# Performance work log

Measured on AMD Instinct MI355X. Metric: run time of the kernel, lower is better.

The kernel has to match this reference:

```python
import jax, jax.numpy as jnp
import numpy as np

N, D = 320, 256
TEMP = 2.0

# case ids sorted: [-11,-10,-1,0,1,10,11]; value order: [0,1,2,3,11,12,13]
CASE_VALS = jnp.array([-11, -10, -1, 0, 1, 10, 11], dtype=jnp.int32)
TABLE = jnp.array([
    [0, 2, 2, 1, 1, 0, 1],   # case -11
    [0, 2, 2, 2, 2, 2, 2],   # case -10
    [0, 2, 2, 2, 1, 0, 2],   # case -1
    [0, 2, 2, 2, 2, 2, 2],   # case 0
    [0, 2, 2, 2, 1, 2, 2],   # case 1
    [0, 2, 2, 2, 2, 0, 2],   # case 10
    [0, 2, 2, 1, 1, 0, 1],   # case 11
], dtype=jnp.int32)


def setup_inputs() -> dict:
    key = jax.random.key(0)
    k1, k2, k3 = jax.random.split(key, 3)
    features = jax.random.normal(k1, (N, D), dtype=jnp.float32)
    y_times = jax.random.uniform(k2, (N,), dtype=jnp.float32)
    y_events = jax.random.randint(k3, (N,), 0, 2, dtype=jnp.int32)
    return {"features": features, "y_times": y_times, "y_events": y_events}


def _forward(features, y_times, y_events):
    n = features.shape[0]
    # pairwise -L2 similarity / temperature  (safe sqrt: diag is 0)
    diff = features[:, None, :] - features[None, :, :]          # [N,N,D]
    d2 = jnp.sum(diff * diff, axis=-1)                           # [N,N]
    norm = jnp.where(d2 > 0, jnp.sqrt(jnp.where(d2 > 0, d2, 1.0)), 0.0)
    logits = -norm / TEMP
    logits = logits - jax.lax.stop_gradient(jnp.max(logits, axis=1, keepdims=True))
    exp_logits = jnp.exp(logits)

    idx = jnp.arange(n)
    eye = idx[:, None] == idx[None, :]

    def per_anchor(k):
        pld = y_times - y_times[k]                               # [N]
        abs_i = jnp.abs(pld)[:, None]                            # |pld[i]|
        pj = pld[None, :]                                        # pld[j]
        # sequential torch mask assignments collapse to this piecewise map
        td = jnp.where(pj > abs_i, 3,
             jnp.where(-pj > abs_i, 1,
             jnp.where(jnp.abs(pj) > 0, 2, 0))).astype(jnp.int32)
        td = jnp.where(eye, 0, td)                               # fill_diagonal_(0)
        neg = jnp.where(td != 0, y_events[None, :] * 10 + td, 0) # {0,1,2,3,11,12,13}
        sgn = jnp.sign(pld).astype(jnp.int32)
        cid = (y_events + 10 * y_events[k]) * sgn                # per-row case id
        cidx = jnp.searchsorted(CASE_VALS, cid)                  # [N]
        vidx = jnp.where(neg > 3, neg - 7, neg)                  # map vals to 0..6
        mapped = TABLE[cidx[:, None], vidx]                      # numba lookup, fused
        final = (mapped == 1).astype(jnp.float32) + 0.5 * (mapped == 2)
        keep = (idx != k).astype(jnp.float32)                    # delete row/col k
        final = final * keep[:, None] * keep[None, :]
        valid = jnp.sum(final, axis=-1) > 0                      # [N]
        Np = jnp.sum(valid)
        denom = jnp.sum(final * exp_logits, axis=-1)             # masked sum-exp
        logp = logits[:, k] - jnp.log(jnp.where(valid, denom, 1.0))
        loss_k = -jnp.sum(jnp.where(valid, logp, 0.0)) / jnp.maximum(Np, 1)
        return jnp.where(Np > 0, loss_k, 0.0), (Np > 0)

    losses, has_pos = jax.vmap(per_anchor)(idx)
    return jnp.sum(losses) / jnp.sum(has_pos)


def reference(features, y_times, y_events):
    return _forward(features, y_times, y_events)
```

## Files before the change

kernel.cpp:

```cpp
#include <hip/hip_runtime.h>
#include <math.h>

#define NN 320
#define DD 256

__device__ __constant__ unsigned int c_PACK[7] =
    {0x2294u, 0x1554u, 0x1254u, 0x1554u, 0x1654u, 0x1154u, 0x2294u};

__global__ __launch_bounds__(256) void prep_kernel(
    const float* __restrict__ F, const float* __restrict__ yt,
    const int* __restrict__ ye, float4* __restrict__ FT4,
    float4* __restrict__ meta, float* __restrict__ acc) {
    __shared__ float sh[64 * 65];
    __shared__ int rr[3][4][64];
    const int b = blockIdx.x;
    const int tid = threadIdx.x;
    if (b < 20) {
        float (*tile)[65] = (float(*)[65])sh;
        const int I = b % 5;
        const int J = b / 5;
        const int lane = tid & 63;
        const int quad = tid >> 6;
#pragma unroll
        for (int r0 = 0; r0 < 64; r0 += 4) {
            const int r = r0 + quad;
            tile[r][lane] = F[(I * 64 + r) * DD + J * 64 + lane];
        }
        __syncthreads();
#pragma unroll
        for (int q = 0; q < 16; q += 4) {
            const int d4 = q + quad;
            float4 v = make_float4(tile[lane][d4 * 4 + 0], tile[lane][d4 * 4 + 1],
                                   tile[lane][d4 * 4 + 2], tile[lane][d4 * 4 + 3]);
            FT4[(J * 16 + d4) * NN + I * 64 + lane] = v;
        }
    } else if (b < 25) {
        float* s_t = sh;
        for (int l = tid; l < NN; l += 256) s_t[l] = yt[l];
        __syncthreads();
        const int jj = tid & 63;
        const int q  = tid >> 6;
        const int j  = (b - 20) * 64 + jj;
        const float tj = s_t[j];
        int lt = 0, le = 0, pos = 0;
        const int l0 = q * 80;
        for (int l = l0; l < l0 + 80; ++l) {
            const float tl = s_t[l];
            lt  += (tl < tj);
            le  += (tl <= tj);
            pos += (tl < tj) || (tl == tj && l < j);
        }
        rr[0][q][jj] = lt; rr[1][q][jj] = le; rr[2][q][jj] = pos;
        __syncthreads();
        if (q == 0) {
#pragma unroll
            for (int w = 1; w < 4; ++w) {
                lt += rr[0][w][jj]; le += rr[1][w][jj]; pos += rr[2][w][jj];
            }
            meta[j] = make_float4(tj, __int_as_float(lt), __int_as_float(le),
                                  __int_as_float(pos | (ye[j] << 16)));
        }
    } else {
        for (int t = tid; t < 2 * NN + 1; t += 256) acc[t] = 0.f;
    }
}

__global__ __launch_bounds__(NN) void fused_kernel(
    const float* __restrict__ F, const float4* __restrict__ FT4,
    const float4* __restrict__ meta, float* __restrict__ acc,
    float* __restrict__ out) {
    __shared__ __align__(16) float fi[DD];
    __shared__ float S0[NN + 1];
    __shared__ float S1[NN + 1];
    __shared__ float w0[5], w1[5];
    __shared__ float4 smi;
    __shared__ int s_done;

    float* __restrict__ accL = acc;
    float* __restrict__ accN = acc + NN;
    unsigned* ticket = (unsigned*)(acc + 2 * NN);

    const int i = blockIdx.x;
    const int j = threadIdx.x;
    const int wave = j >> 6, lane = j & 63;

    if (j < DD) fi[j] = F[i * DD + j];
    if (j == 0) smi = meta[i];
    const float4 mj = meta[j];
    __syncthreads();

    const float4* __restrict__ fi4 = (const float4*)fi;
    float a0 = 0.f, a1 = 0.f, a2 = 0.f, a3 = 0.f;
#pragma unroll 8
    for (int d4 = 0; d4 < DD / 4; ++d4) {
        const float4 f4 = fi4[d4];
        const float4 g4 = FT4[d4 * NN + j];
        const float u0 = f4.x - g4.x, u1 = f4.y - g4.y;
        const float u2 = f4.z - g4.z, u3 = f4.w - g4.w;
        a0 = fmaf(u0, u0, a0);
        a1 = fmaf(u1, u1, a1);
        a2 = fmaf(u2, u2, a2);
        a3 = fmaf(u3, u3, a3);
    }
    const float d2 = (a0 + a1) + (a2 + a3);
    const float nrm = (d2 > 0.f) ? sqrtf(d2) : 0.f;
    const float lg = -0.5f * nrm;
    const float e = expf(lg);

    const int pej = __float_as_int(mj.w);
    const int pos = pej & 0xFFFF;
    const int evj = pej >> 16;
    S0[pos] = evj ? 0.f : e;
    S1[pos] = evj ? e : 0.f;
    __syncthreads();

    float v0 = S0[j], v1 = S1[j];
#pragma unroll
    for (int off = 1; off < 64; off <<= 1) {
        const float n0 = __shfl_up(v0, off);
        const float n1 = __shfl_up(v1, off);
        if (lane >= off) { v0 += n0; v1 += n1; }
    }
    if (lane == 63) { w0[wave] = v0; w1[wave] = v1; }
    __syncthreads();
    float p0 = 0.f, p1 = 0.f;
#pragma unroll
    for (int w = 0; w < 4; ++w) {
        if (wave > w) { p0 += w0[w]; p1 += w1[w]; }
    }
    v0 += p0; v1 += p1;
    S0[j + 1] = v0; S1[j + 1] = v1;
    if (j == 0) { S0[0] = 0.f; S1[0] = 0.f; }
    __syncthreads();

    const float4 mi = smi;
    const float ti = mi.x;
    const int rlt_i = __float_as_int(mi.y), rle_i = __float_as_int(mi.z);
    const int evi   = __float_as_int(mi.w) >> 16;
    const float ta = mj.x;
    const int rlt_a = __float_as_int(mj.y), rle_a = __float_as_int(mj.z);
    const int eva   = evj;

    const int sgn = (ti > ta) ? 1 : ((ti < ta) ? -1 : 0);
    const unsigned pack = c_PACK[3 + sgn * (evi + 2 * eva)];
    const int rlo = min(rlt_i, rlt_a);
    const int rhi = max(rle_i, rle_a);

    const float q0lo = S0[rlo], q0hi = S0[rhi], q0a = S0[rlt_a], q0b = S0[rle_a], t0 = S0[NN];
    const float q1lo = S1[rlo], q1hi = S1[rhi], q1a = S1[rlt_a], q1b = S1[rle_a], t1 = S1[NN];

    const float LO0 = q0lo, HI0 = t0 - q0hi, MI0 = q0hi - q0lo - (q0b - q0a);
    const float LO1 = q1lo, HI1 = t1 - q1hi, MI1 = q1hi - q1lo - (q1b - q1a);

    const float c1 = (float)((pack >> 2) & 3u),  c2 = (float)((pack >> 4) & 3u);
    const float c3 = (float)((pack >> 6) & 3u),  c4 = (float)((pack >> 8) & 3u);
    const float c5 = (float)((pack >> 10) & 3u), c6 = (float)((pack >> 12) & 3u);

    float dx = c1 * LO0 + c2 * MI0 + c3 * HI0 + c4 * LO1 + c5 * MI1 + c6 * HI1;
    if (ti != ta) dx -= (float)((pack >> (2 * (2 + 3 * evi))) & 3u);

    if (i != j && dx > 0.f) {
        atomicAdd(&accL[j], lg - logf(0.5f * dx));
        atomicAdd(&accN[j], 1.f);
    }

    __threadfence();
    __syncthreads();
    if (j == 0) {
        const unsigned old = atomicAdd(ticket, 1u);
        s_done = (old == NN - 1);
    }
    __syncthreads();
    if (!s_done) return;
    __threadfence();

    const float nj = accN[j];
    float lossj = (nj > 0.f) ? (-accL[j] / nj) : 0.f;
    float hasj  = (nj > 0.f) ? 1.f : 0.f;
#pragma unroll
    for (int off = 32; off > 0; off >>= 1) {
        lossj += __shfl_down(lossj, off);
        hasj  += __shfl_down(hasj, off);
    }
    if (lane == 0) { w0[wave] = lossj; w1[wave] = hasj; }
    __syncthreads();
    if (j == 0) {
        float tl = 0.f, th = 0.f;
#pragma unroll
        for (int w = 0; w < 5; ++w) { tl += w0[w]; th += w1[w]; }
        out[0] = tl / th;
    }
}

extern "C" void kernel_launch(void* const* d_in, const int* in_sizes, int n_in,
                              void* d_out, int out_size, void* d_ws, size_t ws_size,
                              hipStream_t stream) {
    const float* F  = (const float*)d_in[0];
    const float* yt = (const float*)d_in[1];
    const int*   ye = (const int*)d_in[2];
    float* out = (float*)d_out;
    float* ws  = (float*)d_ws;

    float4* meta = (float4*)ws;
    float4* FT4  = (float4*)(ws + 4 * NN);
    float*  acc  = ws + 4 * NN + 4 * (DD / 4) * NN;

    prep_kernel<<<26, 256, 0, stream>>>(F, yt, ye, FT4, meta, acc);
    fused_kernel<<<NN, NN, 0, stream>>>(F, FT4, meta, acc, out);
}
```

Baseline: 93.71 us.

## Process two anchor rows per block to reuse transposed feature loads

```diff
diff --git a/kernel.cpp b/kernel.cpp
--- a/kernel.cpp
+++ b/kernel.cpp
@@ -69,106 +69,149 @@
     const float* __restrict__ F, const float4* __restrict__ FT4,
     const float4* __restrict__ meta, float* __restrict__ acc,
     float* __restrict__ out) {
-    __shared__ __align__(16) float fi[DD];
-    __shared__ float S0[NN + 1];
-    __shared__ float S1[NN + 1];
-    __shared__ float w0[5], w1[5];
-    __shared__ float4 smi;
+    __shared__ __align__(16) float fiA[DD];
+    __shared__ __align__(16) float fiB[DD];
+    __shared__ float S0A[NN + 1];
+    __shared__ float S1A[NN + 1];
+    __shared__ float S0B[NN + 1];
+    __shared__ float S1B[NN + 1];
+    __shared__ float wv[4][5];
+    __shared__ float4 smiA, smiB;
     __shared__ int s_done;
 
     float* __restrict__ accL = acc;
     float* __restrict__ accN = acc + NN;
     unsigned* ticket = (unsigned*)(acc + 2 * NN);
 
-    const int i = blockIdx.x;
+    const int i0 = blockIdx.x * 2;
+    const int i1 = i0 + 1;
     const int j = threadIdx.x;
     const int wave = j >> 6, lane = j & 63;
 
-    if (j < DD) fi[j] = F[i * DD + j];
-    if (j == 0) smi = meta[i];
+    if (j < DD) {
+        fiA[j] = F[i0 * DD + j];
+        fiB[j] = F[i1 * DD + j];
+    }
+    if (j == 0) smiA = meta[i0];
+    if (j == 1) smiB = meta[i1];
     const float4 mj = meta[j];
     __syncthreads();
 
-    const float4* __restrict__ fi4 = (const float4*)fi;
-    float a0 = 0.f, a1 = 0.f, a2 = 0.f, a3 = 0.f;
+    const float4* __restrict__ fA4 = (const float4*)fiA;
+    const float4* __restrict__ fB4 = (const float4*)fiB;
+    float aA0 = 0.f, aA1 = 0.f, aA2 = 0.f, aA3 = 0.f;
+    float aB0 = 0.f, aB1 = 0.f, aB2 = 0.f, aB3 = 0.f;
 #pragma unroll 8
     for (int d4 = 0; d4 < DD / 4; ++d4) {
-        const float4 f4 = fi4[d4];
         const float4 g4 = FT4[d4 * NN + j];
-        const float u0 = f4.x - g4.x, u1 = f4.y - g4.y;
-        const float u2 = f4.z - g4.z, u3 = f4.w - g4.w;
-        a0 = fmaf(u0, u0, a0);
-        a1 = fmaf(u1, u1, a1);
-        a2 = fmaf(u2, u2, a2);
-        a3 = fmaf(u3, u3, a3);
-    }
-    const float d2 = (a0 + a1) + (a2 + a3);
-    const float nrm = (d2 > 0.f) ? sqrtf(d2) : 0.f;
-    const float lg = -0.5f * nrm;
-    const float e = expf(lg);
+        const float4 fA = fA4[d4];
+        const float4 fB = fB4[d4];
+        float u;
+        u = fA.x - g4.x; aA0 = fmaf(u, u, aA0);
+        u = fA.y - g4.y; aA1 = fmaf(u, u, aA1);
+        u = fA.z - g4.z; aA2 = fmaf(u, u, aA2);
+        u = fA.w - g4.w; aA3 = fmaf(u, u, aA3);
+        u = fB.x - g4.x; aB0 = fmaf(u, u, aB0);
+        u = fB.y - g4.y; aB1 = fmaf(u, u, aB1);
+        u = fB.z - g4.z; aB2 = fmaf(u, u, aB2);
+        u = fB.w - g4.w; aB3 = fmaf(u, u, aB3);
+    }
+    const float d2A = (aA0 + aA1) + (aA2 + aA3);
+    const float d2B = (aB0 + aB1) + (aB2 + aB3);
+    const float lgA = -0.5f * ((d2A > 0.f) ? sqrtf(d2A) : 0.f);
+    const float lgB = -0.5f * ((d2B > 0.f) ? sqrtf(d2B) : 0.f);
+    const float eA = expf(lgA);
+    const float eB = expf(lgB);
 
     const int pej = __float_as_int(mj.w);
     const int pos = pej & 0xFFFF;
     const int evj = pej >> 16;
-    S0[pos] = evj ? 0.f : e;
-    S1[pos] = evj ? e : 0.f;
-    __syncthreads();
-
-    float v0 = S0[j], v1 = S1[j];
+    S0A[pos] = evj ? 0.f : eA;
+    S1A[pos] = evj ? eA : 0.f;
+    S0B[pos] = evj ? 0.f : eB;
+    S1B[pos] = evj ? eB : 0.f;
+    __syncthreads();
+
+    float vA0 = S0A[j], vA1 = S1A[j], vB0 = S0B[j], vB1 = S1B[j];
 #pragma unroll
     for (int off = 1; off < 64; off <<= 1) {
-        const float n0 = __shfl_up(v0, off);
-        const float n1 = __shfl_up(v1, off);
-        if (lane >= off) { v0 += n0; v1 += n1; }
-    }
-    if (lane == 63) { w0[wave] = v0; w1[wave] = v1; }
-    __syncthreads();
-    float p0 = 0.f, p1 = 0.f;
+        const float nA0 = __shfl_up(vA0, off);
+        const float nA1 = __shfl_up(vA1, off);
+        const float nB0 = __shfl_up(vB0, off);
+        const float nB1 = __shfl_up(vB1, off);
+        if (lane >= off) { vA0 += nA0; vA1 += nA1; vB0 += nB0; vB1 += nB1; }
+    }
+    if (lane == 63) {
+        wv[0][wave] = vA0; wv[1][wave] = vA1;
+        wv[2][wave] = vB0; wv[3][wave] = vB1;
+    }
+    __syncthreads();
+    float pA0 = 0.f, pA1 = 0.f, pB0 = 0.f, pB1 = 0.f;
 #pragma unroll
     for (int w = 0; w < 4; ++w) {
-        if (wave > w) { p0 += w0[w]; p1 += w1[w]; }
-    }
-    v0 += p0; v1 += p1;
-    S0[j + 1] = v0; S1[j + 1] = v1;
-    if (j == 0) { S0[0] = 0.f; S1[0] = 0.f; }
-    __syncthreads();
-
-    const float4 mi = smi;
-    const float ti = mi.x;
-    const int rlt_i = __float_as_int(mi.y), rle_i = __float_as_int(mi.z);
-    const int evi   = __float_as_int(mi.w) >> 16;
+        if (wave > w) {
+            pA0 += wv[0][w]; pA1 += wv[1][w];
+            pB0 += wv[2][w]; pB1 += wv[3][w];
+        }
+    }
+    vA0 += pA0; vA1 += pA1; vB0 += pB0; vB1 += pB1;
+    S0A[j + 1] = vA0; S1A[j + 1] = vA1;
+    S0B[j + 1] = vB0; S1B[j + 1] = vB1;
+    if (j == 0) { S0A[0] = 0.f; S1A[0] = 0.f; S0B[0] = 0.f; S1B[0] = 0.f; }
+    __syncthreads();
+
     const float ta = mj.x;
     const int rlt_a = __float_as_int(mj.y), rle_a = __float_as_int(mj.z);
     const int eva   = evj;
 
-    const int sgn = (ti > ta) ? 1 : ((ti < ta) ? -1 : 0);
-    const unsigned pack = c_PACK[3 + sgn * (evi + 2 * eva)];
-    const int rlo = min(rlt_i, rlt_a);
-    const int rhi = max(rle_i, rle_a);
-
-    const float q0lo = S0[rlo], q0hi = S0[rhi], q0a = S0[rlt_a], q0b = S0[rle_a], t0 = S0[NN];
-    const float q1lo = S1[rlo], q1hi = S1[rhi], q1a = S1[rlt_a], q1b = S1[rle_a], t1 = S1[NN];
-
-    const float LO0 = q0lo, HI0 = t0 - q0hi, MI0 = q0hi - q0lo - (q0b - q0a);
-    const float LO1 = q1lo, HI1 = t1 - q1hi, MI1 = q1hi - q1lo - (q1b - q1a);
-
-    const float c1 = (float)((pack >> 2) & 3u),  c2 = (float)((pack >> 4) & 3u);
-    const float c3 = (float)((pack >> 6) & 3u),  c4 = (float)((pack >> 8) & 3u);
-    const float c5 = (float)((pack >> 10) & 3u), c6 = (float)((pack >> 12) & 3u);
-
-    float dx = c1 * LO0 + c2 * MI0 + c3 * HI0 + c4 * LO1 + c5 * MI1 + c6 * HI1;
-    if (ti != ta) dx -= (float)((pack >> (2 * (2 + 3 * evi))) & 3u);
-
-    if (i != j && dx > 0.f) {
-        atomicAdd(&accL[j], lg - logf(0.5f * dx));
-        atomicAdd(&accN[j], 1.f);
+    float lp = 0.f, np = 0.f;
+#pragma unroll
+    for (int r = 0; r < 2; ++r) {
+        const float4 mi = (r == 0) ? smiA : smiB;
+        const float* __restrict__ S0 = (r == 0) ? S0A : S0B;
+        const float* __restrict__ S1 = (r == 0) ? S1A : S1B;
+        const float lg = (r == 0) ? lgA : lgB;
+        const int irow = (r == 0) ? i0 : i1;
+
+        const float ti = mi.x;
+        const int rlt_i = __float_as_int(mi.y), rle_i = __float_as_int(mi.z);
+        const int evi   = __float_as_int(mi.w) >> 16;
+
+        const int sgn = (ti > ta) ? 1 : ((ti < ta) ? -1 : 0);
+        const unsigned pack = c_PACK[3 + sgn * (evi + 2 * eva)];
+        const int rlo = min(rlt_i, rlt_a);
+        const int rhi = max(rle_i, rle_a);
+
+        const float q0lo = S0[rlo], q0hi = S0[rhi];
+        const float q0a = S0[rlt_a], q0b = S0[rle_a], t0 = S0[NN];
+        const float q1lo = S1[rlo], q1hi = S1[rhi];
+        const float q1a = S1[rlt_a], q1b = S1[rle_a], t1 = S1[NN];
+
+        const float LO0 = q0lo, HI0 = t0 - q0hi, MI0 = q0hi - q0lo - (q0b - q0a);
+        const float LO1 = q1lo, HI1 = t1 - q1hi, MI1 = q1hi - q1lo - (q1b - q1a);
+
+        const float c1 = (float)((pack >> 2) & 3u),  c2 = (float)((pack >> 4) & 3u);
+        const float c3 = (float)((pack >> 6) & 3u),  c4 = (float)((pack >> 8) & 3u);
+        const float c5 = (float)((pack >> 10) & 3u), c6 = (float)((pack >> 12) & 3u);
+
+        float dx = c1 * LO0 + c2 * MI0 + c3 * HI0 + c4 * LO1 + c5 * MI1 + c6 * HI1;
+        if (ti != ta) dx -= (float)((pack >> (2 * (2 + 3 * evi))) & 3u);
+
+        if (irow != j && dx > 0.f) {
+            lp += lg - logf(0.5f * dx);
+            np += 1.f;
+        }
+    }
+    if (np > 0.f) {
+        atomicAdd(&accL[j], lp);
+        atomicAdd(&accN[j], np);
     }
 
     __threadfence();
     __syncthreads();
     if (j == 0) {
         const unsigned old = atomicAdd(ticket, 1u);
-        s_done = (old == NN - 1);
+        s_done = (old == (NN / 2) - 1);
     }
     __syncthreads();
     if (!s_done) return;
@@ -182,12 +225,12 @@
         lossj += __shfl_down(lossj, off);
         hasj  += __shfl_down(hasj, off);
     }
-    if (lane == 0) { w0[wave] = lossj; w1[wave] = hasj; }
+    if (lane == 0) { wv[0][wave] = lossj; wv[1][wave] = hasj; }
     __syncthreads();
     if (j == 0) {
         float tl = 0.f, th = 0.f;
 #pragma unroll
-        for (int w = 0; w < 5; ++w) { tl += w0[w]; th += w1[w]; }
+        for (int w = 0; w < 5; ++w) { tl += wv[0][w]; th += wv[1][w]; }
         out[0] = tl / th;
     }
 }
@@ -206,5 +249,5 @@
     float*  acc  = ws + 4 * NN + 4 * (DD / 4) * NN;
 
     prep_kernel<<<26, 256, 0, stream>>>(F, yt, ye, FT4, meta, acc);
-    fused_kernel<<<NN, NN, 0, stream>>>(F, FT4, meta, acc, out);
+    fused_kernel<<<NN / 2, NN, 0, stream>>>(F, FT4, meta, acc, out);
 }
```

After: 81.90 us. 12.6% less time.
